# Performance work log

Measured on AMD Instinct MI355X. Metric: run time of the kernel, lower is better.

## Reference

```python
import jax, jax.numpy as jnp
import numpy as np

NA, NB = 40000, 40000
D_IN, D_OUT, H, C = 256, 256, 8, 32  # C = D_OUT // H
E = 400000
N_MP = 3


def setup_inputs() -> dict:
    key = jax.random.key(0)
    ks = jax.random.split(key, 16)
    s = 1.0 / np.sqrt(D_IN)
    inp = {
        "x_A": jax.random.normal(ks[0], (NA, D_IN), jnp.float32),
        "x_B": jax.random.normal(ks[1], (NB, D_IN), jnp.float32),
        "edge_ab": jax.random.randint(ks[2], (2, E), 0, NB, jnp.int32),  # src in A, dst in B
        "edge_ba": jax.random.randint(ks[3], (2, E), 0, NA, jnp.int32),  # src in B, dst in A
        "edge_aa": jax.random.randint(ks[4], (2, E), 0, NA, jnp.int32),  # src in A, dst in A
        "W_A": jax.random.normal(ks[5], (D_IN, D_OUT), jnp.float32) * s,
        "b_A": jnp.zeros((D_OUT,), jnp.float32),
        "W_B": jax.random.normal(ks[6], (D_IN, D_OUT), jnp.float32) * s,
        "b_B": jnp.zeros((D_OUT,), jnp.float32),
        "attn_l": jax.random.normal(ks[7], (N_MP, H, C), jnp.float32) * 0.1,
        "attn_r": jax.random.normal(ks[8], (N_MP, H, C), jnp.float32) * 0.1,
        "rel_l_A": jax.random.normal(ks[9], (H, C), jnp.float32) * 0.1,
        "rel_r_A": jax.random.normal(ks[10], (H, C), jnp.float32) * 0.1,
        "rel_l_B": jax.random.normal(ks[11], (H, C), jnp.float32) * 0.1,
        "rel_r_B": jax.random.normal(ks[12], (H, C), jnp.float32) * 0.1,
    }
    return inp


def _leaky(x):
    return jax.nn.leaky_relu(x, negative_slope=0.2)


def _gat_relation(h_src, edge, a_l, a_r, n_dst):
    """GAT-style edge attention + segment softmax + scatter-add.
    h_src: [N_src,H,C], edge: [2,E], a_l: [N_src,H], a_r: [N_dst,H]."""
    src, dst = edge[0], edge[1]
    e = _leaky(a_l[src] + a_r[dst])                      # [E,H]
    m = jax.ops.segment_max(e, dst, num_segments=n_dst)  # [N_dst,H]
    ex = jnp.exp(e - m[dst])
    denom = jax.ops.segment_sum(ex, dst, num_segments=n_dst)
    alpha = ex / denom[dst]                              # softmax over in-neighbors
    msg = h_src[src] * alpha[:, :, None]                 # [E,H,C]
    return jax.ops.segment_sum(msg, dst, num_segments=n_dst)  # [N_dst,H,C]


def _beta_combine(h, rel_embs, rel_l, rel_r):
    """Relation-level attention (get_beta_weights) + weighted sum.
    h: [N,H,C], rel_embs: [N,H,R,C]."""
    bl = (h * rel_l).sum(-1)                                 # [N,H]
    br = (rel_embs * rel_r[None, :, None, :]).sum(-1)        # [N,H,R]
    beta = jax.nn.softmax(_leaky(bl[:, :, None] + br), axis=2)
    out = (rel_embs * beta[..., None]).sum(2)                # [N,H,C]
    return out.reshape(out.shape[0], H * C)


def reference(x_A, x_B, edge_ab, edge_ba, edge_aa, W_A, b_A, W_B, b_B,
              attn_l, attn_r, rel_l_A, rel_r_A, rel_l_B, rel_r_B):
    nA, nB = x_A.shape[0], x_B.shape[0]
    h_A = (x_A @ W_A + b_A).reshape(nA, H, C)
    h_B = (x_B @ W_B + b_B).reshape(nB, H, C)

    # per-metapath node attention scalars (get_alphas)
    # metapath 0: A->B, 1: B->A, 2: A->A
    al0 = (h_A * attn_l[0]).sum(-1); ar0 = (h_B * attn_r[0]).sum(-1)
    al1 = (h_B * attn_l[1]).sum(-1); ar1 = (h_A * attn_r[1]).sum(-1)
    al2 = (h_A * attn_l[2]).sum(-1); ar2 = (h_A * attn_r[2]).sum(-1)

    # aggregate per tail relation (agg_relation_neighbors); last slot = self
    rel_ba = _gat_relation(h_B, edge_ba, al1, ar1, nA)
    rel_aa = _gat_relation(h_A, edge_aa, al2, ar2, nA)
    emb_A = jnp.stack([rel_ba, rel_aa, h_A], axis=2)         # [NA,H,3,C]

    rel_ab = _gat_relation(h_A, edge_ab, al0, ar0, nB)
    emb_B = jnp.stack([rel_ab, h_B], axis=2)                 # [NB,H,2,C]

    out_A = jax.nn.relu(_beta_combine(h_A, emb_A, rel_l_A, rel_r_A))
    out_B = jax.nn.relu(_beta_combine(h_B, emb_B, rel_l_B, rel_r_B))
    return jnp.concatenate([out_A, out_B], axis=0)           # [NA+NB, D_OUT]
```

## Files before the change

kernel.cpp:

```cpp
#include <hip/hip_runtime.h>
#include <math.h>

#define NAn 40000
#define NBn 40000
#define DIN 256
#define DOUT 256
#define NH 8
#define NC 32
#define NE 400000
#define CAP 64

typedef __attribute__((ext_vector_type(8))) short short8;
typedef __attribute__((ext_vector_type(4))) float floatx4;

__device__ __forceinline__ float leaky(float x) { return x > 0.f ? x : 0.2f * x; }
__device__ __forceinline__ float dot4(float4 a, float4 b) {
  return a.x * b.x + a.y * b.y + a.z * b.z + a.w * b.w;
}
__device__ __forceinline__ unsigned bf16_rne_bits(float x) {
  unsigned u = __float_as_uint(x);
  unsigned r = u + 0x7fffu + ((u >> 16) & 1u);
  return r & 0xffff0000u;
}
__device__ __forceinline__ float4 bf4(uint2 u) {
  float4 f;
  f.x = __uint_as_float(u.x << 16);
  f.y = __uint_as_float(u.x & 0xffff0000u);
  f.z = __uint_as_float(u.y << 16);
  f.w = __uint_as_float(u.y & 0xffff0000u);
  return f;
}
__device__ __forceinline__ void bf8(uint4 u, float* f) {
  f[0] = __uint_as_float(u.x << 16);
  f[1] = __uint_as_float(u.x & 0xffff0000u);
  f[2] = __uint_as_float(u.y << 16);
  f[3] = __uint_as_float(u.y & 0xffff0000u);
  f[4] = __uint_as_float(u.z << 16);
  f[5] = __uint_as_float(u.z & 0xffff0000u);
  f[6] = __uint_as_float(u.w << 16);
  f[7] = __uint_as_float(u.w & 0xffff0000u);
}

__global__ void wswz(const float* __restrict__ WA, const float* __restrict__ WB,
                     short8* __restrict__ hiA, short8* __restrict__ hiB,
                     int* __restrict__ cnts) {
  int t = blockIdx.x * blockDim.x + threadIdx.x;
  for (int i = t; i < 3 * NAn; i += 16384) cnts[i] = 0;
  const float* W;
  short8* hi;
  int tt = t;
  if (tt < 8192) {
    W = WA; hi = hiA;
  } else {
    tt -= 8192;
    if (tt >= 8192) return;
    W = WB; hi = hiB;
  }
  int kt = tt >> 10, nt = (tt >> 6) & 15, l = tt & 63;
  int n = nt * 16 + (l & 15);
  int kb = kt * 32 + (l >> 4) * 8;
  short8 h8;
#pragma unroll
  for (int j = 0; j < 8; ++j) {
    float w = W[(size_t)(kb + j) * DOUT + n];
    h8[j] = (short)(bf16_rne_bits(w) >> 16);
  }
  hi[tt] = h8;
}

__global__ __launch_bounds__(256) void gemm_mfma(
    const float* __restrict__ XA, const float* __restrict__ XB,
    const short8* __restrict__ WAhi, const short8* __restrict__ WBhi,
    const float* __restrict__ bA, const float* __restrict__ bB,
    unsigned* __restrict__ HAbf, unsigned* __restrict__ HBbf) {
  __shared__ short8 bfrag[2][1024];
  int blk = blockIdx.x;
  const float* X;
  const short8* Wh;
  const float* bias;
  unsigned* Hbf;
  if (blk < NAn / 64) {
    X = XA; Wh = WAhi; bias = bA; Hbf = HAbf;
  } else {
    blk -= NAn / 64;
    X = XB; Wh = WBhi; bias = bB; Hbf = HBbf;
  }
  const int tid = threadIdx.x;
  const int lane = tid & 63, wave = tid >> 6;
  const int row0 = blk * 64 + wave * 16;
  const int col16 = lane & 15, quad = lane >> 4;

  floatx4 acc[16];
#pragma unroll
  for (int i = 0; i < 16; ++i) acc[i] = (floatx4){0.f, 0.f, 0.f, 0.f};

  const float4* xp = (const float4*)(X + (size_t)(row0 + col16) * DIN) + quad * 2;

  uint4 pre[4];
  const uint4* wsrc = (const uint4*)Wh;
#pragma unroll
  for (int c = 0; c < 4; ++c) pre[c] = wsrc[c * 256 + tid];
  {
    uint4* d = (uint4*)&bfrag[0][0];
#pragma unroll
    for (int c = 0; c < 4; ++c) d[c * 256 + tid] = pre[c];
  }
  __syncthreads();

  for (int kt = 0; kt < 8; ++kt) {
    if (kt < 7) {
      const uint4* s = wsrc + (size_t)(kt + 1) * 1024;
#pragma unroll
      for (int c = 0; c < 4; ++c) pre[c] = s[c * 256 + tid];
    }
    float4 x0 = xp[kt * 8];
    float4 x1 = xp[kt * 8 + 1];
    float xv[8] = {x0.x, x0.y, x0.z, x0.w, x1.x, x1.y, x1.z, x1.w};
    short8 ahi, alo;
#pragma unroll
    for (int j = 0; j < 8; ++j) {
      unsigned hb = bf16_rne_bits(xv[j]);
      ahi[j] = (short)(hb >> 16);
      float rem = xv[j] - __uint_as_float(hb);
      alo[j] = (short)(bf16_rne_bits(rem) >> 16);
    }
    const short8* bp = &bfrag[kt & 1][0];
#pragma unroll
    for (int nt = 0; nt < 16; ++nt) {
      short8 bv = bp[nt * 64 + lane];
      acc[nt] = __builtin_amdgcn_mfma_f32_16x16x32_bf16(ahi, bv, acc[nt], 0, 0, 0);
      acc[nt] = __builtin_amdgcn_mfma_f32_16x16x32_bf16(alo, bv, acc[nt], 0, 0, 0);
    }
    if (kt < 7) {
      uint4* d = (uint4*)&bfrag[(kt + 1) & 1][0];
#pragma unroll
      for (int c = 0; c < 4; ++c) d[c * 256 + tid] = pre[c];
    }
    __syncthreads();
  }
#pragma unroll
  for (int nt = 0; nt < 16; ++nt) {
    float bcol = bias[nt * 16 + col16];
#pragma unroll
    for (int r = 0; r < 4; ++r) {
      int row = row0 + quad * 4 + r;
      float v = acc[nt][r] + bcol;
      float vp = __shfl_xor(v, 1);
      if ((lane & 1) == 0) {
        unsigned p = (bf16_rne_bits(v) >> 16) | bf16_rne_bits(vp);
        Hbf[(size_t)row * 128 + nt * 8 + (col16 >> 1)] = p;
      }
    }
  }
}

__global__ void alphas(const uint2* __restrict__ hAbf, const uint2* __restrict__ hBbf,
                       const float* __restrict__ attn_l, const float* __restrict__ attn_r,
                       float* __restrict__ al0, float* __restrict__ ar1,
                       float* __restrict__ al2, float* __restrict__ ar2,
                       float* __restrict__ ar0, float* __restrict__ al1) {
  int idx = blockIdx.x * blockDim.x + threadIdx.x;
  if (idx >= (NAn + NBn) * NH) return;
  bool isA = idx < NAn * NH;
  int k = isA ? idx : idx - NAn * NH;
  int head = k & 7;
  const uint2* h8 = (isA ? hAbf : hBbf) + (size_t)k * 8;
  if (isA) {
    const float4* l0 = (const float4*)(attn_l + 0 * DOUT + head * NC);
    const float4* r1 = (const float4*)(attn_r + 1 * DOUT + head * NC);
    const float4* l2 = (const float4*)(attn_l + 2 * DOUT + head * NC);
    const float4* r2 = (const float4*)(attn_r + 2 * DOUT + head * NC);
    float s0 = 0, s1 = 0, s2 = 0, s3 = 0;
#pragma unroll
    for (int q = 0; q < 8; ++q) {
      float4 hv = bf4(h8[q]);
      s0 += dot4(hv, l0[q]);
      s1 += dot4(hv, r1[q]);
      s2 += dot4(hv, l2[q]);
      s3 += dot4(hv, r2[q]);
    }
    al0[k] = s0;
    ar1[k] = s1;
    al2[k] = s2;
    ar2[k] = s3;
  } else {
    const float4* r0 = (const float4*)(attn_r + 0 * DOUT + head * NC);
    const float4* l1 = (const float4*)(attn_l + 1 * DOUT + head * NC);
    float s0 = 0, s1 = 0;
#pragma unroll
    for (int q = 0; q < 8; ++q) {
      float4 hv = bf4(h8[q]);
      s0 += dot4(hv, r0[q]);
      s1 += dot4(hv, l1[q]);
    }
    ar0[k] = s0;
    al1[k] = s1;
  }
}

__global__ void build_csr3(const int* __restrict__ e_ba, const int* __restrict__ e_aa,
                           const int* __restrict__ e_ab, int* __restrict__ cnt_ba,
                           int* __restrict__ cnt_aa, int* __restrict__ cnt_ab,
                           int* __restrict__ sl_ba, int* __restrict__ sl_aa,
                           int* __restrict__ sl_ab) {
  int i = blockIdx.x * blockDim.x + threadIdx.x;
  if (i >= 3 * NE) return;
  const int* e;
  int* cnt;
  int* sl;
  int k = i;
  if (i < NE) {
    e = e_ba; cnt = cnt_ba; sl = sl_ba;
  } else if (i < 2 * NE) {
    e = e_aa; cnt = cnt_aa; sl = sl_aa; k = i - NE;
  } else {
    e = e_ab; cnt = cnt_ab; sl = sl_ab; k = i - 2 * NE;
  }
  int src = e[k];
  int dst = e[NE + k];
  int pos = atomicAdd(&cnt[dst], 1);
  if (pos < CAP) sl[(size_t)dst * CAP + pos] = src;
}

__device__ __forceinline__ void gat2(int dst, int wave, int lane, int h, int sub, int head,
                                     const int* __restrict__ cnt,
                                     const int* __restrict__ slots,
                                     const float* __restrict__ al,
                                     const float* __restrict__ ar,
                                     const uint4* __restrict__ hbf,
                                     int lds_slot[4][64], float lds_ex[4][512],
                                     float acc[8]) {
#pragma unroll
  for (int k = 0; k < 8; ++k) acc[k] = 0.f;
  int deg = cnt[dst];
  if (deg > CAP) deg = CAP;
  if (deg == 0) return;
  __threadfence_block();
  if (lane < deg) {
    int s = slots[(size_t)dst * CAP + lane];
    lds_slot[wave][lane] = s;
    float4 a0 = *(const float4*)(al + (size_t)s * 8);
    float4 a1 = *(const float4*)(al + (size_t)s * 8 + 4);
    float4 r0 = *(const float4*)(ar + (size_t)dst * 8);
    float4 r1 = *(const float4*)(ar + (size_t)dst * 8 + 4);
    float* exq = &lds_ex[wave][lane * 8];
    exq[0] = __expf(leaky(a0.x + r0.x));
    exq[1] = __expf(leaky(a0.y + r0.y));
    exq[2] = __expf(leaky(a0.z + r0.z));
    exq[3] = __expf(leaky(a0.w + r0.w));
    exq[4] = __expf(leaky(a1.x + r1.x));
    exq[5] = __expf(leaky(a1.y + r1.y));
    exq[6] = __expf(leaky(a1.z + r1.z));
    exq[7] = __expf(leaky(a1.w + r1.w));
  }
  __threadfence_block();
  float den = 0.f;
  int j = h;
  if (j < deg) {
    int sj = lds_slot[wave][j];
    float w = lds_ex[wave][j * 8 + head];
    uint4 u = hbf[(size_t)sj * 32 + sub];
    while (true) {
      uint4 cu = u;
      float cw = w;
      int jn = j + 2;
      if (jn < deg) {
        int sn = lds_slot[wave][jn];
        w = lds_ex[wave][jn * 8 + head];
        u = hbf[(size_t)sn * 32 + sub];
      }
      den += cw;
      float f[8];
      bf8(cu, f);
#pragma unroll
      for (int k = 0; k < 8; ++k) acc[k] += cw * f[k];
      j = jn;
      if (j >= deg) break;
    }
  }
#pragma unroll
  for (int k = 0; k < 8; ++k) acc[k] += __shfl_xor(acc[k], 32);
  den += __shfl_xor(den, 32);
  float inv = 1.f / den;
#pragma unroll
  for (int k = 0; k < 8; ++k) acc[k] *= inv;
}

__global__ __launch_bounds__(256) void agg_combine(
    const int* __restrict__ cnt_ba, const int* __restrict__ sl_ba,
    const float* __restrict__ al1, const float* __restrict__ ar1,
    const int* __restrict__ cnt_aa, const int* __restrict__ sl_aa,
    const float* __restrict__ al2, const float* __restrict__ ar2,
    const int* __restrict__ cnt_ab, const int* __restrict__ sl_ab,
    const float* __restrict__ al0, const float* __restrict__ ar0,
    const uint4* __restrict__ hAbf, const uint4* __restrict__ hBbf,
    const float* __restrict__ rlA, const float* __restrict__ rrA,
    const float* __restrict__ rlB, const float* __restrict__ rrB,
    float* __restrict__ outp) {
  __shared__ int lds_slot[4][64];
  __shared__ float lds_ex[4][512];
  int wave = threadIdx.x >> 6, lane = threadIdx.x & 63;
  int h = lane >> 5, sub = lane & 31, head = sub >> 2;
  bool isA = blockIdx.x < (NAn / 4);
  int dst = (isA ? blockIdx.x : blockIdx.x - NAn / 4) * 4 + wave;
  float m0[8], hv[8], o[8];
  if (isA) {
    float m1[8];
    gat2(dst, wave, lane, h, sub, head, cnt_ba, sl_ba, al1, ar1, hBbf, lds_slot, lds_ex, m0);
    gat2(dst, wave, lane, h, sub, head, cnt_aa, sl_aa, al2, ar2, hAbf, lds_slot, lds_ex, m1);
    uint4 us = hAbf[(size_t)dst * 32 + sub];
    bf8(us, hv);
    const float4* rl4 = (const float4*)rlA;
    const float4* rr4 = (const float4*)rrA;
    float4 rl0 = rl4[sub * 2], rl1 = rl4[sub * 2 + 1];
    float4 rr0 = rr4[sub * 2], rr1 = rr4[sub * 2 + 1];
    float rl8[8] = {rl0.x, rl0.y, rl0.z, rl0.w, rl1.x, rl1.y, rl1.z, rl1.w};
    float rr8[8] = {rr0.x, rr0.y, rr0.z, rr0.w, rr1.x, rr1.y, rr1.z, rr1.w};
    float pbl = 0, p0 = 0, p1 = 0, p2 = 0;
#pragma unroll
    for (int k = 0; k < 8; ++k) {
      pbl += hv[k] * rl8[k];
      p0 += m0[k] * rr8[k];
      p1 += m1[k] * rr8[k];
      p2 += hv[k] * rr8[k];
    }
#pragma unroll
    for (int d = 1; d < 4; d <<= 1) {
      pbl += __shfl_xor(pbl, d);
      p0 += __shfl_xor(p0, d);
      p1 += __shfl_xor(p1, d);
      p2 += __shfl_xor(p2, d);
    }
    float b0 = leaky(pbl + p0), b1 = leaky(pbl + p1), b2 = leaky(pbl + p2);
    float mx = fmaxf(b0, fmaxf(b1, b2));
    float w0 = __expf(b0 - mx), w1 = __expf(b1 - mx), w2 = __expf(b2 - mx);
    float inv = 1.f / (w0 + w1 + w2);
    w0 *= inv; w1 *= inv; w2 *= inv;
#pragma unroll
    for (int k = 0; k < 8; ++k)
      o[k] = fmaxf(0.f, m0[k] * w0 + m1[k] * w1 + hv[k] * w2);
  } else {
    gat2(dst, wave, lane, h, sub, head, cnt_ab, sl_ab, al0, ar0, hAbf, lds_slot, lds_ex, m0);
    uint4 us = hBbf[(size_t)dst * 32 + sub];
    bf8(us, hv);
    const float4* rl4 = (const float4*)rlB;
    const float4* rr4 = (const float4*)rrB;
    float4 rl0 = rl4[sub * 2], rl1 = rl4[sub * 2 + 1];
    float4 rr0 = rr4[sub * 2], rr1 = rr4[sub * 2 + 1];
    float rl8[8] = {rl0.x, rl0.y, rl0.z, rl0.w, rl1.x, rl1.y, rl1.z, rl1.w};
    float rr8[8] = {rr0.x, rr0.y, rr0.z, rr0.w, rr1.x, rr1.y, rr1.z, rr1.w};
    float pbl = 0, p0 = 0, p1 = 0;
#pragma unroll
    for (int k = 0; k < 8; ++k) {
      pbl += hv[k] * rl8[k];
      p0 += m0[k] * rr8[k];
      p1 += hv[k] * rr8[k];
    }
#pragma unroll
    for (int d = 1; d < 4; d <<= 1) {
      pbl += __shfl_xor(pbl, d);
      p0 += __shfl_xor(p0, d);
      p1 += __shfl_xor(p1, d);
    }
    float b0 = leaky(pbl + p0), b1 = leaky(pbl + p1);
    float mx = fmaxf(b0, b1);
    float w0 = __expf(b0 - mx), w1 = __expf(b1 - mx);
    float inv = 1.f / (w0 + w1);
    w0 *= inv; w1 *= inv;
#pragma unroll
    for (int k = 0; k < 8; ++k) o[k] = fmaxf(0.f, m0[k] * w0 + hv[k] * w1);
  }
  float* orow = outp + (size_t)(isA ? dst : NAn + dst) * DOUT + sub * 8;
  if (h == 0) {
    *(float4*)orow = (float4){o[0], o[1], o[2], o[3]};
    *(float4*)(orow + 4) = (float4){o[4], o[5], o[6], o[7]};
  }
}

extern "C" void kernel_launch(void* const* d_in, const int* in_sizes, int n_in, void* d_out,
                              int out_size, void* d_ws, size_t ws_size, hipStream_t stream) {
  const float* xA = (const float*)d_in[0];
  const float* xB = (const float*)d_in[1];
  const int* e_ab = (const int*)d_in[2];
  const int* e_ba = (const int*)d_in[3];
  const int* e_aa = (const int*)d_in[4];
  const float* WA = (const float*)d_in[5];
  const float* bA = (const float*)d_in[6];
  const float* WB = (const float*)d_in[7];
  const float* bB = (const float*)d_in[8];
  const float* attn_l = (const float*)d_in[9];
  const float* attn_r = (const float*)d_in[10];
  const float* rlA = (const float*)d_in[11];
  const float* rrA = (const float*)d_in[12];
  const float* rlB = (const float*)d_in[13];
  const float* rrB = (const float*)d_in[14];
  float* out = (float*)d_out;

  char* p = (char*)d_ws;
  auto alloc = [&](size_t bytes) -> char* {
    char* r = p;
    p += (bytes + 255) & ~(size_t)255;
    return r;
  };
  unsigned* hAbf = (unsigned*)alloc((size_t)NAn * DOUT * 2);
  unsigned* hBbf = (unsigned*)alloc((size_t)NBn * DOUT * 2);
  float* al0 = (float*)alloc((size_t)NAn * NH * 4);
  float* ar1 = (float*)alloc((size_t)NAn * NH * 4);
  float* al2 = (float*)alloc((size_t)NAn * NH * 4);
  float* ar2 = (float*)alloc((size_t)NAn * NH * 4);
  float* ar0 = (float*)alloc((size_t)NBn * NH * 4);
  float* al1 = (float*)alloc((size_t)NBn * NH * 4);
  short8* WAhi = (short8*)alloc((size_t)8192 * 16);
  short8* WBhi = (short8*)alloc((size_t)8192 * 16);
  int* cnts = (int*)alloc((size_t)3 * NAn * 4);
  int* cnt_ba = cnts;
  int* cnt_aa = cnts + NAn;
  int* cnt_ab = cnts + 2 * NAn;
  int* slots_ba = (int*)alloc((size_t)NAn * CAP * 4);
  int* slots_aa = (int*)alloc((size_t)NAn * CAP * 4);
  int* slots_ab = (int*)alloc((size_t)NBn * CAP * 4);

  wswz<<<64, 256, 0, stream>>>(WA, WB, WAhi, WBhi, cnts);
  build_csr3<<<(3 * NE + 255) / 256, 256, 0, stream>>>(e_ba, e_aa, e_ab, cnt_ba, cnt_aa,
                                                       cnt_ab, slots_ba, slots_aa, slots_ab);
  gemm_mfma<<<(NAn + NBn) / 64, 256, 0, stream>>>(xA, xB, WAhi, WBhi, bA, bB, hAbf, hBbf);
  alphas<<<((NAn + NBn) * NH + 255) / 256, 256, 0, stream>>>(
      (const uint2*)hAbf, (const uint2*)hBbf, attn_l, attn_r, al0, ar1, al2, ar2, ar0, al1);
  agg_combine<<<(NAn + NBn) / 4, 256, 0, stream>>>(
      cnt_ba, slots_ba, al1, ar1, cnt_aa, slots_aa, al2, ar2, cnt_ab, slots_ab, al0, ar0,
      (const uint4*)hAbf, (const uint4*)hBbf, rlA, rrA, rlB, rrB, out);
}
```

Measured before the change: 437.8 us.

## Issue both relations' neighbor loads up front to overlap gather latency

In the aggregation kernel, the per-node GAT work for both incoming relations is now restructured so that degree counts, slot lists, attention scalars, self features and the first neighbor feature rows are all loaded before either accumulation loop runs. Per-relation LDS buffers let both relations' exponentials be staged at once, and slot indices are clamped so every lane can load unconditionally. The aim is more memory-level parallelism and less serialized latency between the two gathers. The cost is extra LDS, more registers and wasted loads for unused lanes beyond the degree.

```diff
diff --git a/kernel.cpp b/kernel.cpp
--- a/kernel.cpp
+++ b/kernel.cpp
@@ -222,51 +222,31 @@
   if (pos < CAP) sl[(size_t)dst * CAP + pos] = src;
 }
 
-__device__ __forceinline__ void gat2(int dst, int wave, int lane, int h, int sub, int head,
-                                     const int* __restrict__ cnt,
-                                     const int* __restrict__ slots,
-                                     const float* __restrict__ al,
-                                     const float* __restrict__ ar,
-                                     const uint4* __restrict__ hbf,
-                                     int lds_slot[4][64], float lds_ex[4][512],
-                                     float acc[8]) {
-#pragma unroll
-  for (int k = 0; k < 8; ++k) acc[k] = 0.f;
-  int deg = cnt[dst];
-  if (deg > CAP) deg = CAP;
-  if (deg == 0) return;
-  __threadfence_block();
-  if (lane < deg) {
-    int s = slots[(size_t)dst * CAP + lane];
-    lds_slot[wave][lane] = s;
-    float4 a0 = *(const float4*)(al + (size_t)s * 8);
-    float4 a1 = *(const float4*)(al + (size_t)s * 8 + 4);
-    float4 r0 = *(const float4*)(ar + (size_t)dst * 8);
-    float4 r1 = *(const float4*)(ar + (size_t)dst * 8 + 4);
-    float* exq = &lds_ex[wave][lane * 8];
-    exq[0] = __expf(leaky(a0.x + r0.x));
-    exq[1] = __expf(leaky(a0.y + r0.y));
-    exq[2] = __expf(leaky(a0.z + r0.z));
-    exq[3] = __expf(leaky(a0.w + r0.w));
-    exq[4] = __expf(leaky(a1.x + r1.x));
-    exq[5] = __expf(leaky(a1.y + r1.y));
-    exq[6] = __expf(leaky(a1.z + r1.z));
-    exq[7] = __expf(leaky(a1.w + r1.w));
-  }
-  __threadfence_block();
-  float den = 0.f;
+__device__ __forceinline__ void exp8(float4 a0, float4 a1, float4 r0, float4 r1,
+                                     float* ex) {
+  ex[0] = __expf(leaky(a0.x + r0.x));
+  ex[1] = __expf(leaky(a0.y + r0.y));
+  ex[2] = __expf(leaky(a0.z + r0.z));
+  ex[3] = __expf(leaky(a0.w + r0.w));
+  ex[4] = __expf(leaky(a1.x + r1.x));
+  ex[5] = __expf(leaky(a1.y + r1.y));
+  ex[6] = __expf(leaky(a1.z + r1.z));
+  ex[7] = __expf(leaky(a1.w + r1.w));
+}
+
+__device__ __forceinline__ void gatloop(int deg, int wave, int ridx, int h, int sub,
+                                        int head, const uint4* __restrict__ hbf,
+                                        int lds_slot[4][2][64], float lds_ex[4][2][512],
+                                        uint4 u, float w, float acc[8], float& den) {
   int j = h;
   if (j < deg) {
-    int sj = lds_slot[wave][j];
-    float w = lds_ex[wave][j * 8 + head];
-    uint4 u = hbf[(size_t)sj * 32 + sub];
     while (true) {
       uint4 cu = u;
       float cw = w;
       int jn = j + 2;
       if (jn < deg) {
-        int sn = lds_slot[wave][jn];
-        w = lds_ex[wave][jn * 8 + head];
+        int sn = lds_slot[wave][ridx][jn];
+        w = lds_ex[wave][ridx][jn * 8 + head];
         u = hbf[(size_t)sn * 32 + sub];
       }
       den += cw;
@@ -281,9 +261,11 @@
 #pragma unroll
   for (int k = 0; k < 8; ++k) acc[k] += __shfl_xor(acc[k], 32);
   den += __shfl_xor(den, 32);
-  float inv = 1.f / den;
-#pragma unroll
-  for (int k = 0; k < 8; ++k) acc[k] *= inv;
+  if (deg > 0) {
+    float inv = 1.f / den;
+#pragma unroll
+    for (int k = 0; k < 8; ++k) acc[k] *= inv;
+  }
 }
 
 __global__ __launch_bounds__(256) void agg_combine(
@@ -297,8 +279,8 @@
     const float* __restrict__ rlA, const float* __restrict__ rrA,
     const float* __restrict__ rlB, const float* __restrict__ rrB,
     float* __restrict__ outp) {
-  __shared__ int lds_slot[4][64];
-  __shared__ float lds_ex[4][512];
+  __shared__ int lds_slot[4][2][64];
+  __shared__ float lds_ex[4][2][512];
   int wave = threadIdx.x >> 6, lane = threadIdx.x & 63;
   int h = lane >> 5, sub = lane & 31, head = sub >> 2;
   bool isA = blockIdx.x < (NAn / 4);
@@ -306,9 +288,44 @@
   float m0[8], hv[8], o[8];
   if (isA) {
     float m1[8];
-    gat2(dst, wave, lane, h, sub, head, cnt_ba, sl_ba, al1, ar1, hBbf, lds_slot, lds_ex, m0);
-    gat2(dst, wave, lane, h, sub, head, cnt_aa, sl_aa, al2, ar2, hAbf, lds_slot, lds_ex, m1);
+    int deg0 = cnt_ba[dst];
+    int deg1 = cnt_aa[dst];
+    int s0 = sl_ba[(size_t)dst * CAP + lane];
+    int s1 = sl_aa[(size_t)dst * CAP + lane];
     uint4 us = hAbf[(size_t)dst * 32 + sub];
+    const float4* ar1_4 = (const float4*)ar1;
+    const float4* ar2_4 = (const float4*)ar2;
+    float4 r00 = ar1_4[dst * 2], r01 = ar1_4[dst * 2 + 1];
+    float4 r10 = ar2_4[dst * 2], r11 = ar2_4[dst * 2 + 1];
+    int s0c = min(max(s0, 0), NBn - 1);
+    int s1c = min(max(s1, 0), NAn - 1);
+    const float4* al1_4 = (const float4*)al1;
+    const float4* al2_4 = (const float4*)al2;
+    float4 a00 = al1_4[(size_t)s0c * 2], a01 = al1_4[(size_t)s0c * 2 + 1];
+    float4 a10 = al2_4[(size_t)s1c * 2], a11 = al2_4[(size_t)s1c * 2 + 1];
+    deg0 = min(deg0, CAP);
+    deg1 = min(deg1, CAP);
+    float ex0[8], ex1[8];
+    exp8(a00, a01, r00, r01, ex0);
+    exp8(a10, a11, r10, r11, ex1);
+    lds_slot[wave][0][lane] = s0c;
+    lds_slot[wave][1][lane] = s1c;
+    *(float4*)&lds_ex[wave][0][lane * 8] = (float4){ex0[0], ex0[1], ex0[2], ex0[3]};
+    *(float4*)&lds_ex[wave][0][lane * 8 + 4] = (float4){ex0[4], ex0[5], ex0[6], ex0[7]};
+    *(float4*)&lds_ex[wave][1][lane * 8] = (float4){ex1[0], ex1[1], ex1[2], ex1[3]};
+    *(float4*)&lds_ex[wave][1][lane * 8 + 4] = (float4){ex1[4], ex1[5], ex1[6], ex1[7]};
+    __threadfence_block();
+    int sj0 = lds_slot[wave][0][h];
+    float w0 = lds_ex[wave][0][h * 8 + head];
+    uint4 u0 = hBbf[(size_t)sj0 * 32 + sub];
+    int sj1 = lds_slot[wave][1][h];
+    float w1 = lds_ex[wave][1][h * 8 + head];
+    uint4 u1 = hAbf[(size_t)sj1 * 32 + sub];
+    float den0 = 0.f, den1 = 0.f;
+#pragma unroll
+    for (int k = 0; k < 8; ++k) { m0[k] = 0.f; m1[k] = 0.f; }
+    gatloop(deg0, wave, 0, h, sub, head, hBbf, lds_slot, lds_ex, u0, w0, m0, den0);
+    gatloop(deg1, wave, 1, h, sub, head, hAbf, lds_slot, lds_ex, u1, w1, m1, den1);
     bf8(us, hv);
     const float4* rl4 = (const float4*)rlA;
     const float4* rr4 = (const float4*)rrA;
@@ -333,15 +350,35 @@
     }
     float b0 = leaky(pbl + p0), b1 = leaky(pbl + p1), b2 = leaky(pbl + p2);
     float mx = fmaxf(b0, fmaxf(b1, b2));
-    float w0 = __expf(b0 - mx), w1 = __expf(b1 - mx), w2 = __expf(b2 - mx);
-    float inv = 1.f / (w0 + w1 + w2);
-    w0 *= inv; w1 *= inv; w2 *= inv;
+    float w0b = __expf(b0 - mx), w1b = __expf(b1 - mx), w2b = __expf(b2 - mx);
+    float inv = 1.f / (w0b + w1b + w2b);
+    w0b *= inv; w1b *= inv; w2b *= inv;
 #pragma unroll
     for (int k = 0; k < 8; ++k)
-      o[k] = fmaxf(0.f, m0[k] * w0 + m1[k] * w1 + hv[k] * w2);
+      o[k] = fmaxf(0.f, m0[k] * w0b + m1[k] * w1b + hv[k] * w2b);
   } else {
-    gat2(dst, wave, lane, h, sub, head, cnt_ab, sl_ab, al0, ar0, hAbf, lds_slot, lds_ex, m0);
+    int deg0 = cnt_ab[dst];
+    int s0 = sl_ab[(size_t)dst * CAP + lane];
     uint4 us = hBbf[(size_t)dst * 32 + sub];
+    const float4* ar0_4 = (const float4*)ar0;
+    float4 r00 = ar0_4[dst * 2], r01 = ar0_4[dst * 2 + 1];
+    int s0c = min(max(s0, 0), NAn - 1);
+    const float4* al0_4 = (const float4*)al0;
+    float4 a00 = al0_4[(size_t)s0c * 2], a01 = al0_4[(size_t)s0c * 2 + 1];
+    deg0 = min(deg0, CAP);
+    float ex0[8];
+    exp8(a00, a01, r00, r01, ex0);
+    lds_slot[wave][0][lane] = s0c;
+    *(float4*)&lds_ex[wave][0][lane * 8] = (float4){ex0[0], ex0[1], ex0[2], ex0[3]};
+    *(float4*)&lds_ex[wave][0][lane * 8 + 4] = (float4){ex0[4], ex0[5], ex0[6], ex0[7]};
+    __threadfence_block();
+    int sj0 = lds_slot[wave][0][h];
+    float w0 = lds_ex[wave][0][h * 8 + head];
+    uint4 u0 = hAbf[(size_t)sj0 * 32 + sub];
+    float den0 = 0.f;
+#pragma unroll
+    for (int k = 0; k < 8; ++k) m0[k] = 0.f;
+    gatloop(deg0, wave, 0, h, sub, head, hAbf, lds_slot, lds_ex, u0, w0, m0, den0);
     bf8(us, hv);
     const float4* rl4 = (const float4*)rlB;
     const float4* rr4 = (const float4*)rrB;
@@ -364,11 +401,11 @@
     }
     float b0 = leaky(pbl + p0), b1 = leaky(pbl + p1);
     float mx = fmaxf(b0, b1);
-    float w0 = __expf(b0 - mx), w1 = __expf(b1 - mx);
-    float inv = 1.f / (w0 + w1);
-    w0 *= inv; w1 *= inv;
-#pragma unroll
-    for (int k = 0; k < 8; ++k) o[k] = fmaxf(0.f, m0[k] * w0 + hv[k] * w1);
+    float w0b = __expf(b0 - mx), w1b = __expf(b1 - mx);
+    float inv = 1.f / (w0b + w1b);
+    w0b *= inv; w1b *= inv;
+#pragma unroll
+    for (int k = 0; k < 8; ++k) o[k] = fmaxf(0.f, m0[k] * w0b + hv[k] * w1b);
   }
   float* orow = outp + (size_t)(isA ? dst : NAn + dst) * DOUT + sub * 8;
   if (h == 0) {
```

Result: no change. 439.2 us (+0.3%).
